# Performance work log

Hardware: AMD Instinct MI355X
Metric: run time of the kernel (lower is better)

Reference implementation:

```python
import jax, jax.numpy as jnp
import numpy as np

N_NODES = 50000
N_EDGES = 800000
NFEAT, NHID, NCLASS = 512, 256, 128
N_UV = 2048


def gcn_layer(x, adj_row, adj_col, adj_val, W, b):
    # support = x @ W ; out = A @ support (sparse COO spmm) + b
    support = x @ W                                   # [N, out]
    msgs = adj_val[:, None] * support[adj_col]        # [E, out]
    out = jax.ops.segment_sum(msgs, adj_row, num_segments=N_NODES)
    return out + b


def setup_inputs() -> dict:
    key = jax.random.key(0)
    ks = jax.random.split(key, 12)
    u = jax.random.randint(ks[0], (N_UV,), 0, N_NODES)
    v = jax.random.randint(ks[1], (N_UV,), 0, N_NODES)
    x = jax.random.normal(ks[2], (N_NODES, NFEAT), dtype=jnp.float32)
    adj_row = jnp.sort(jax.random.randint(ks[3], (N_EDGES,), 0, N_NODES))
    adj_col = jax.random.randint(ks[4], (N_EDGES,), 0, N_NODES)
    adj_val = jax.random.uniform(ks[5], (N_EDGES,), dtype=jnp.float32)
    s1 = 1.0 / np.sqrt(NHID)
    s2 = 1.0 / np.sqrt(NCLASS)
    W1 = jax.random.uniform(ks[6], (NFEAT, NHID), minval=-s1, maxval=s1, dtype=jnp.float32)
    b1 = jax.random.uniform(ks[7], (NHID,), minval=-s1, maxval=s1, dtype=jnp.float32)
    W2 = jax.random.uniform(ks[8], (NHID, NCLASS), minval=-s2, maxval=s2, dtype=jnp.float32)
    b2 = jax.random.uniform(ks[9], (NCLASS,), minval=-s2, maxval=s2, dtype=jnp.float32)
    We = jax.random.normal(ks[10], (NCLASS, NCLASS), dtype=jnp.float32) * (1.0 / np.sqrt(NCLASS))
    return {"u": u, "v": v, "x": x, "adj_row": adj_row, "adj_col": adj_col,
            "adj_val": adj_val, "W1": W1, "b1": b1, "W2": W2, "b2": b2, "We": We}


def reference(u, v, x, adj_row, adj_col, adj_val, W1, b1, W2, b2, We):
    # layer 1: GCN + ReLU (dropout is identity in eval mode)
    h = jax.nn.relu(gcn_layer(x, adj_row, adj_col, adj_val, W1, b1))
    # layer 2: GCN
    z = gcn_layer(h, adj_row, adj_col, adj_val, W2, b2)          # [N, nclass]
    # edge scoring: sigmoid(w_edge(z[u]) @ z[v].T)
    zu = z[u] @ We.T                                             # [U, nclass] (nn.Linear: x @ W.T)
    zv = z[v]                                                    # [V, nclass]
    p_uv = jax.nn.sigmoid(zu @ zv.T)                             # [U, V]
    return p_uv
```

## Files before the change

### kernel.cpp

```cpp
#include <hip/hip_runtime.h>
#include <hip/hip_bf16.h>
#include <math.h>

#define N_NODES 50000
#define N_EDGES 800000
#define NFEAT   512
#define NHID    256
#define NCLASS  128
#define N_UV    2048

#define Q24_SCALE  524288.0f
#define Q24_INV    1.9073486328125e-6f

typedef __bf16    bf16x8 __attribute__((ext_vector_type(8)));
typedef short     s16x8  __attribute__((ext_vector_type(8)));
typedef float     f32x4  __attribute__((ext_vector_type(4)));

struct __attribute__((packed)) U3 { unsigned a, b, c; };

__device__ __forceinline__ unsigned short bf16_rn(float f) {
  unsigned u = __float_as_uint(f);
  u += 0x7fffu + ((u >> 16) & 1u);
  return (unsigned short)(u >> 16);
}
__device__ __forceinline__ float bf16_to_f(unsigned short h) {
  return __uint_as_float(((unsigned)h) << 16);
}
__device__ __forceinline__ void unpack24(unsigned a, unsigned b, unsigned c,
                                         int& e0, int& e1, int& e2, int& e3) {
  e0 = ((int)(a << 8)) >> 8;
  e1 = ((int)((b << 16) | ((a >> 24) << 8))) >> 8;
  e2 = ((int)((c << 24) | ((b >> 16) << 8))) >> 8;
  e3 = ((int)c) >> 8;
}

#define LDSPAD 72

template <bool ASPLIT, int OMODE>
__global__ __launch_bounds__(256, 4) void gemm_mfma_wide(
    const float* __restrict__ Af,
    const unsigned short* __restrict__ Ahi, const unsigned short* __restrict__ Alo,
    const unsigned short* __restrict__ BThi, const unsigned short* __restrict__ BTlo,
    float* __restrict__ C, unsigned char* __restrict__ Cq, int M, int N, int K) {
  __shared__ unsigned short sAh[64 * LDSPAD];
  __shared__ unsigned short sAl[64 * LDSPAD];

  const int tid  = threadIdx.x;
  const int lane = tid & 63;
  const int wave = tid >> 6;
  const int wn   = wave << 5;
  const int lm   = lane & 15;
  const int quad = lane >> 4;
  const int m0   = blockIdx.y * 64;
  const int n0   = blockIdx.x * 128;

  const int r32 = tid >> 4;
  const int c32 = (tid & 15) * 4;
  const int r16 = tid >> 3;
  const int c16 = (tid & 7) * 8;

  float4 pA[4]; s16x8 pAh[2], pAl[2];

  f32x4 acc[4][2];
#pragma unroll
  for (int i = 0; i < 4; ++i)
#pragma unroll
    for (int j = 0; j < 2; ++j)
#pragma unroll
      for (int r = 0; r < 4; ++r) acc[i][j][r] = 0.f;

#define LOAD_TILE(k0)                                                          \
  do {                                                                         \
    if (ASPLIT) {                                                              \
      _Pragma("unroll") for (int p = 0; p < 4; ++p) {                          \
        const int m = m0 + p * 16 + r32;                                       \
        pA[p] = make_float4(0.f, 0.f, 0.f, 0.f);                               \
        if (m < M) pA[p] = *(const float4*)&Af[(size_t)m * K + (k0) + c32];    \
      }                                                                        \
    } else {                                                                   \
      _Pragma("unroll") for (int p = 0; p < 2; ++p) {                          \
        const int m = m0 + p * 32 + r16;                                       \
        _Pragma("unroll") for (int e = 0; e < 8; ++e) { pAh[p][e] = 0; pAl[p][e] = 0; } \
        if (m < M) {                                                           \
          pAh[p] = *(const s16x8*)&Ahi[(size_t)m * K + (k0) + c16];            \
          pAl[p] = *(const s16x8*)&Alo[(size_t)m * K + (k0) + c16];            \
        }                                                                      \
      }                                                                        \
    }                                                                          \
  } while (0)

#define SPLIT4W(v, hv, lv)                                                     \
  hv.x = bf16_rn(v.x); lv.x = bf16_rn(v.x - bf16_to_f(hv.x));                  \
  hv.y = bf16_rn(v.y); lv.y = bf16_rn(v.y - bf16_to_f(hv.y));                  \
  hv.z = bf16_rn(v.z); lv.z = bf16_rn(v.z - bf16_to_f(hv.z));                  \
  hv.w = bf16_rn(v.w); lv.w = bf16_rn(v.w - bf16_to_f(hv.w));

#define STORE_TILE()                                                           \
  do {                                                                         \
    if (ASPLIT) {                                                              \
      _Pragma("unroll") for (int p = 0; p < 4; ++p) {                          \
        ushort4 hv, lv; SPLIT4W(pA[p], hv, lv);                                \
        const int row = p * 16 + r32;                                          \
        *(ushort4*)&sAh[row * LDSPAD + c32] = hv;                              \
        *(ushort4*)&sAl[row * LDSPAD + c32] = lv;                              \
      }                                                                        \
    } else {                                                                   \
      _Pragma("unroll") for (int p = 0; p < 2; ++p) {                          \
        const int row = p * 32 + r16;                                          \
        *(s16x8*)&sAh[row * LDSPAD + c16] = pAh[p];                            \
        *(s16x8*)&sAl[row * LDSPAD + c16] = pAl[p];                            \
      }                                                                        \
    }                                                                          \
  } while (0)

  LOAD_TILE(0);

  const unsigned short* Bhrow = BThi + (size_t)(n0 + wn + lm) * K;
  const unsigned short* Blrow = BTlo + (size_t)(n0 + wn + lm) * K;

  for (int k0 = 0; k0 < K; k0 += 64) {
    if (k0) __syncthreads();
    STORE_TILE();
    __syncthreads();

    bf16x8 bH[2][2], bL[2][2];
#pragma unroll
    for (int ks = 0; ks < 2; ++ks)
#pragma unroll
      for (int j = 0; j < 2; ++j) {
        const size_t off = (size_t)(j * 16) * K + k0 + ks * 32 + quad * 8;
        bH[ks][j] = __builtin_bit_cast(bf16x8, *(const s16x8*)(Bhrow + off));
        bL[ks][j] = __builtin_bit_cast(bf16x8, *(const s16x8*)(Blrow + off));
      }

    if (k0 + 64 < K) LOAD_TILE(k0 + 64);

#pragma unroll
    for (int ks = 0; ks < 2; ++ks) {
      const int koff = ks * 32 + quad * 8;
#pragma unroll
      for (int i = 0; i < 4; ++i) {
        const int r = i * 16 + lm;
        const bf16x8 aH = __builtin_bit_cast(bf16x8, *(const s16x8*)&sAh[r * LDSPAD + koff]);
        const bf16x8 aL = __builtin_bit_cast(bf16x8, *(const s16x8*)&sAl[r * LDSPAD + koff]);
#pragma unroll
        for (int j = 0; j < 2; ++j) {
          acc[i][j] = __builtin_amdgcn_mfma_f32_16x16x32_bf16(aH, bH[ks][j], acc[i][j], 0, 0, 0);
          acc[i][j] = __builtin_amdgcn_mfma_f32_16x16x32_bf16(aH, bL[ks][j], acc[i][j], 0, 0, 0);
          acc[i][j] = __builtin_amdgcn_mfma_f32_16x16x32_bf16(aL, bH[ks][j], acc[i][j], 0, 0, 0);
        }
      }
    }
  }

#pragma unroll
  for (int i = 0; i < 4; ++i)
#pragma unroll
    for (int j = 0; j < 2; ++j) {
      const int col = n0 + wn + j * 16 + lm;
#pragma unroll
      for (int r = 0; r < 4; ++r) {
        const int row = m0 + i * 16 + quad * 4 + r;
        if (row < M) {
          float v = acc[i][j][r];
          if (OMODE == 2) {
            int q = __float2int_rn(v * Q24_SCALE);
            q = q > 8388607 ? 8388607 : (q < -8388608 ? -8388608 : q);
            unsigned char* p = Cq + ((size_t)row * N + col) * 3;
            p[0] = (unsigned char)(q & 0xFF);
            p[1] = (unsigned char)((q >> 8) & 0xFF);
            p[2] = (unsigned char)((q >> 16) & 0xFF);
          } else {
            C[(size_t)row * N + col] = v;
          }
        }
      }
    }
#undef LOAD_TILE
#undef STORE_TILE
#undef SPLIT4W
}

template <int OMODE>
__global__ __launch_bounds__(256, 2) void gemm_mfma_split(
    const float* __restrict__ Af, const float* __restrict__ BTf,
    float* __restrict__ C, int M, int N, int K) {
  __shared__ unsigned short sAh[128 * LDSPAD];
  __shared__ unsigned short sAl[128 * LDSPAD];
  __shared__ unsigned short sBh[128 * LDSPAD];
  __shared__ unsigned short sBl[128 * LDSPAD];

  const int tid  = threadIdx.x;
  const int lane = tid & 63;
  const int wave = tid >> 6;
  const int wm   = (wave >> 1) << 6;
  const int wn   = (wave & 1) << 6;
  const int lm   = lane & 15;
  const int quad = lane >> 4;
  const int m0   = blockIdx.y * 128;
  const int n0   = blockIdx.x * 128;

  const int r32 = tid >> 4;
  const int c32 = (tid & 15) * 4;

  float4 pA[8];
  float4 pB[8];

  f32x4 acc[4][4];
#pragma unroll
  for (int i = 0; i < 4; ++i)
#pragma unroll
    for (int j = 0; j < 4; ++j)
#pragma unroll
      for (int r = 0; r < 4; ++r) acc[i][j][r] = 0.f;

#define LOAD_TILE(k0)                                                          \
  do {                                                                         \
    _Pragma("unroll") for (int p = 0; p < 8; ++p) {                            \
      const int m = m0 + p * 16 + r32;                                         \
      pA[p] = make_float4(0.f, 0.f, 0.f, 0.f);                                 \
      if (m < M) pA[p] = *(const float4*)&Af[(size_t)m * K + (k0) + c32];      \
    }                                                                          \
    _Pragma("unroll") for (int p = 0; p < 8; ++p) {                            \
      const int n = n0 + p * 16 + r32;                                         \
      pB[p] = *(const float4*)&BTf[(size_t)n * K + (k0) + c32];                \
    }                                                                          \
  } while (0)

#define SPLIT4(v, hv, lv)                                                      \
  hv.x = bf16_rn(v.x); lv.x = bf16_rn(v.x - bf16_to_f(hv.x));                  \
  hv.y = bf16_rn(v.y); lv.y = bf16_rn(v.y - bf16_to_f(hv.y));                  \
  hv.z = bf16_rn(v.z); lv.z = bf16_rn(v.z - bf16_to_f(hv.z));                  \
  hv.w = bf16_rn(v.w); lv.w = bf16_rn(v.w - bf16_to_f(hv.w));

#define STORE_TILE()                                                           \
  do {                                                                         \
    _Pragma("unroll") for (int p = 0; p < 8; ++p) {                            \
      ushort4 hv, lv; SPLIT4(pA[p], hv, lv);                                   \
      const int row = p * 16 + r32;                                            \
      *(ushort4*)&sAh[row * LDSPAD + c32] = hv;                                \
      *(ushort4*)&sAl[row * LDSPAD + c32] = lv;                                \
    }                                                                          \
    _Pragma("unroll") for (int p = 0; p < 8; ++p) {                            \
      ushort4 hv, lv; SPLIT4(pB[p], hv, lv);                                   \
      const int row = p * 16 + r32;                                            \
      *(ushort4*)&sBh[row * LDSPAD + c32] = hv;                                \
      *(ushort4*)&sBl[row * LDSPAD + c32] = lv;                                \
    }                                                                          \
  } while (0)

  LOAD_TILE(0);

  for (int k0 = 0; k0 < K; k0 += 64) {
    if (k0) __syncthreads();
    STORE_TILE();
    __syncthreads();
    if (k0 + 64 < K) LOAD_TILE(k0 + 64);

#pragma unroll
    for (int ks = 0; ks < 2; ++ks) {
      const int koff = ks * 32 + quad * 8;
      bf16x8 aH[4], aL[4], bH[4], bL[4];
#pragma unroll
      for (int i = 0; i < 4; ++i) {
        const int r = wm + i * 16 + lm;
        aH[i] = __builtin_bit_cast(bf16x8, *(const s16x8*)&sAh[r * LDSPAD + koff]);
        aL[i] = __builtin_bit_cast(bf16x8, *(const s16x8*)&sAl[r * LDSPAD + koff]);
      }
#pragma unroll
      for (int j = 0; j < 4; ++j) {
        const int r = wn + j * 16 + lm;
        bH[j] = __builtin_bit_cast(bf16x8, *(const s16x8*)&sBh[r * LDSPAD + koff]);
        bL[j] = __builtin_bit_cast(bf16x8, *(const s16x8*)&sBl[r * LDSPAD + koff]);
      }
#pragma unroll
      for (int i = 0; i < 4; ++i)
#pragma unroll
        for (int j = 0; j < 4; ++j) {
          acc[i][j] = __builtin_amdgcn_mfma_f32_16x16x32_bf16(aH[i], bH[j], acc[i][j], 0, 0, 0);
          acc[i][j] = __builtin_amdgcn_mfma_f32_16x16x32_bf16(aH[i], bL[j], acc[i][j], 0, 0, 0);
          acc[i][j] = __builtin_amdgcn_mfma_f32_16x16x32_bf16(aL[i], bH[j], acc[i][j], 0, 0, 0);
        }
    }
  }

#pragma unroll
  for (int i = 0; i < 4; ++i)
#pragma unroll
    for (int j = 0; j < 4; ++j) {
      const int col = n0 + wn + j * 16 + lm;
#pragma unroll
      for (int r = 0; r < 4; ++r) {
        const int row = m0 + wm + i * 16 + quad * 4 + r;
        if (row < M) {
          float v = acc[i][j][r];
          if (OMODE == 1) v = 1.f / (1.f + expf(-v));
          C[(size_t)row * N + col] = v;
        }
      }
    }
#undef LOAD_TILE
#undef STORE_TILE
#undef SPLIT4
}

__global__ __launch_bounds__(256) void prep_all(
    const int* __restrict__ rows, int* __restrict__ row_ptr,
    const float* __restrict__ W1, unsigned short* __restrict__ W1Thi,
    unsigned short* __restrict__ W1Tlo,
    const float* __restrict__ W2, unsigned short* __restrict__ W2Thi,
    unsigned short* __restrict__ W2Tlo) {
  const int idx = blockIdx.x * 256 + threadIdx.x;
  if (idx < N_EDGES) {
    const int r = rows[idx];
    const int rprev = (idx == 0) ? -1 : rows[idx - 1];
    for (int n = rprev + 1; n <= r; ++n) row_ptr[n] = idx;
    if (idx == N_EDGES - 1)
      for (int n = r + 1; n <= N_NODES; ++n) row_ptr[n] = N_EDGES;
  }
  if (idx < NFEAT * NHID) {
    const int n = idx / NFEAT;
    const int k = idx - n * NFEAT;
    const float f = W1[(size_t)k * NHID + n];
    const unsigned short h = bf16_rn(f);
    W1Thi[idx] = h;
    W1Tlo[idx] = bf16_rn(f - bf16_to_f(h));
  }
  if (idx < NHID * NCLASS) {
    const int n = idx / NHID;
    const int k = idx - n * NHID;
    const float f = W2[(size_t)k * NCLASS + n];
    const unsigned short h = bf16_rn(f);
    W2Thi[idx] = h;
    W2Tlo[idx] = bf16_rn(f - bf16_to_f(h));
  }
}

__global__ __launch_bounds__(256, 4) void spmm256_q24_split(
    const unsigned char* __restrict__ Sq, const int* __restrict__ row_ptr,
    const int* __restrict__ cols, const float* __restrict__ vals,
    const float4* __restrict__ bias4,
    unsigned short* __restrict__ outHi, unsigned short* __restrict__ outLo) {
  const int wave = threadIdx.x >> 6;
  const int lane = threadIdx.x & 63;
  const int node = blockIdx.x * 4 + wave;

  const int lou = __builtin_amdgcn_readfirstlane(row_ptr[node]);
  const int hiu = __builtin_amdgcn_readfirstlane(row_ptr[node + 1]);

  float4 acc = make_float4(0.f, 0.f, 0.f, 0.f);
  const int lane12 = lane * 12;

  for (int base = lou; base < hiu; base += 16) {
    int   c[16];
    float w[16];
    if (base + 16 <= hiu) {
#pragma unroll
      for (int t = 0; t < 16; ++t) {
        c[t] = cols[base + t];
        w[t] = vals[base + t] * Q24_INV;
      }
    } else {
#pragma unroll
      for (int t = 0; t < 16; ++t) {
        const int idx = base + t;
        const int ide = idx < hiu ? idx : hiu - 1;
        c[t] = cols[ide];
        w[t] = idx < hiu ? vals[ide] * Q24_INV : 0.f;
      }
    }
    U3 d[16];
#pragma unroll
    for (int t = 0; t < 16; ++t)
      d[t] = *(const U3*)&Sq[(size_t)c[t] * (NHID * 3) + lane12];
#pragma unroll
    for (int t = 0; t < 16; ++t) {
      int e0, e1, e2, e3;
      unpack24(d[t].a, d[t].b, d[t].c, e0, e1, e2, e3);
      acc.x = fmaf(w[t], (float)e0, acc.x);
      acc.y = fmaf(w[t], (float)e1, acc.y);
      acc.z = fmaf(w[t], (float)e2, acc.z);
      acc.w = fmaf(w[t], (float)e3, acc.w);
    }
  }

  const float4 b = bias4[lane];
  acc.x = fmaxf(acc.x + b.x, 0.f);
  acc.y = fmaxf(acc.y + b.y, 0.f);
  acc.z = fmaxf(acc.z + b.z, 0.f);
  acc.w = fmaxf(acc.w + b.w, 0.f);

  ushort4 hv, lv;
  hv.x = bf16_rn(acc.x); lv.x = bf16_rn(acc.x - bf16_to_f(hv.x));
  hv.y = bf16_rn(acc.y); lv.y = bf16_rn(acc.y - bf16_to_f(hv.y));
  hv.z = bf16_rn(acc.z); lv.z = bf16_rn(acc.z - bf16_to_f(hv.z));
  hv.w = bf16_rn(acc.w); lv.w = bf16_rn(acc.w - bf16_to_f(hv.w));
  const size_t o = (size_t)node * NHID + lane * 4;
  *(ushort4*)&outHi[o] = hv;
  *(ushort4*)&outLo[o] = lv;
}

__global__ __launch_bounds__(256) void spmm128_f32_list(
    const float4* __restrict__ S4, const int* __restrict__ row_ptr,
    const int* __restrict__ cols, const float* __restrict__ vals,
    const float4* __restrict__ bias4,
    const int* __restrict__ u, const int* __restrict__ v,
    float4* __restrict__ out4) {
  const int wave = threadIdx.x >> 6;
  const int lane = threadIdx.x & 63;
  const int half = lane >> 5;
  const int l32  = lane & 31;
  const int idx  = blockIdx.x * 4 + wave;
  const int node = idx < N_UV ? u[idx] : v[idx - N_UV];

  const int lo = row_ptr[node];
  const int hi = row_ptr[node + 1];

  float4 acc = make_float4(0.f, 0.f, 0.f, 0.f);
  int e = lo + half;
  for (; e + 6 < hi; e += 8) {
    int c[4]; float w[4];
#pragma unroll
    for (int t = 0; t < 4; ++t) { c[t] = cols[e + 2 * t]; w[t] = vals[e + 2 * t]; }
    float4 r[4];
#pragma unroll
    for (int t = 0; t < 4; ++t) r[t] = S4[(size_t)c[t] * 32 + l32];
#pragma unroll
    for (int t = 0; t < 4; ++t) {
      acc.x = fmaf(w[t], r[t].x, acc.x); acc.y = fmaf(w[t], r[t].y, acc.y);
      acc.z = fmaf(w[t], r[t].z, acc.z); acc.w = fmaf(w[t], r[t].w, acc.w);
    }
  }
  for (; e < hi; e += 2) {
    const int c = cols[e];
    const float w = vals[e];
    const float4 r = S4[(size_t)c * 32 + l32];
    acc.x = fmaf(w, r.x, acc.x); acc.y = fmaf(w, r.y, acc.y);
    acc.z = fmaf(w, r.z, acc.z); acc.w = fmaf(w, r.w, acc.w);
  }

  acc.x += __shfl_xor(acc.x, 32);
  acc.y += __shfl_xor(acc.y, 32);
  acc.z += __shfl_xor(acc.z, 32);
  acc.w += __shfl_xor(acc.w, 32);

  if (half == 0) {
    const float4 b = bias4[l32];
    acc.x += b.x; acc.y += b.y; acc.z += b.z; acc.w += b.w;
    out4[(size_t)idx * 32 + l32] = acc;
  }
}

extern "C" void kernel_launch(void* const* d_in, const int* in_sizes, int n_in,
                              void* d_out, int out_size, void* d_ws, size_t ws_size,
                              hipStream_t stream) {
  const int*   u       = (const int*)  d_in[0];
  const int*   v       = (const int*)  d_in[1];
  const float* x       = (const float*)d_in[2];
  const int*   adj_row = (const int*)  d_in[3];
  const int*   adj_col = (const int*)  d_in[4];
  const float* adj_val = (const float*)d_in[5];
  const float* W1      = (const float*)d_in[6];
  const float* b1      = (const float*)d_in[7];
  const float* W2      = (const float*)d_in[8];
  const float* b2      = (const float*)d_in[9];
  const float* We      = (const float*)d_in[10];
  float* out = (float*)d_out;

  char* wsb = (char*)d_ws;
  unsigned char* S1q = (unsigned char*)wsb;
  float* S2  = (float*)wsb;
  float* ZUV = (float*)(wsb + (size_t)N_NODES * NCLASS * sizeof(float));
  char* rB = wsb + (size_t)N_NODES * NHID * sizeof(float);
  unsigned short* Hhi = (unsigned short*)rB;
  unsigned short* Hlo = Hhi + (size_t)N_NODES * NHID;
  float* ZU = (float*)rB;
  unsigned short* W1Thi = (unsigned short*)out;
  unsigned short* W1Tlo = W1Thi + NHID * NFEAT;
  unsigned short* W2Thi = W1Tlo + NHID * NFEAT;
  unsigned short* W2Tlo = W2Thi + NCLASS * NHID;
  int* row_ptr = (int*)(W2Tlo + NCLASS * NHID);

  prep_all<<<(N_EDGES + 255) / 256, 256, 0, stream>>>(
      adj_row, row_ptr, W1, W1Thi, W1Tlo, W2, W2Thi, W2Tlo);

  gemm_mfma_wide<true, 2>
      <<<dim3(NHID / 128, (N_NODES + 63) / 64), 256, 0, stream>>>(
      x, nullptr, nullptr, W1Thi, W1Tlo,
      nullptr, S1q, N_NODES, NHID, NFEAT);

  spmm256_q24_split<<<N_NODES / 4, 256, 0, stream>>>(
      S1q, row_ptr, adj_col, adj_val, (const float4*)b1, Hhi, Hlo);

  gemm_mfma_wide<false, 0>
      <<<dim3(NCLASS / 128, (N_NODES + 63) / 64), 256, 0, stream>>>(
      nullptr, Hhi, Hlo, W2Thi, W2Tlo,
      S2, nullptr, N_NODES, NCLASS, NHID);

  spmm128_f32_list<<<(2 * N_UV) / 4, 256, 0, stream>>>(
      (const float4*)S2, row_ptr, adj_col, adj_val, (const float4*)b2,
      u, v, (float4*)ZUV);

  gemm_mfma_split<0>
      <<<dim3(NCLASS / 128, N_UV / 128), 256, 0, stream>>>(
      ZUV, We, ZU, N_UV, NCLASS, NCLASS);

  gemm_mfma_split<1>
      <<<dim3(N_UV / 128, N_UV / 128), 256, 0, stream>>>(
      ZU, ZUV + (size_t)N_UV * NCLASS, out, N_UV, N_UV, NCLASS);
}
```

Before: 370.2 us.

## Reorder layer-2 as aggregate-then-transform only for needed u/v nodes

Layer 2 used to run the H·W2 GEMM over all 50000 nodes and then gather only 4096 u/v rows. It now aggregates the 256-wide H for just those 4096 nodes, then multiplies the small result by W2 with the bias fused into the epilogue. This drops a full-graph GEMM and the bf16 hi/lo split of H. In exchange H is stored as fp32 (more bytes written by the first SpMM), and the second aggregation gathers 256-wide rows instead of 128-wide.

```diff
diff --git a/kernel.cpp b/kernel.cpp
--- a/kernel.cpp
+++ b/kernel.cpp
@@ -41,7 +41,8 @@
     const float* __restrict__ Af,
     const unsigned short* __restrict__ Ahi, const unsigned short* __restrict__ Alo,
     const unsigned short* __restrict__ BThi, const unsigned short* __restrict__ BTlo,
-    float* __restrict__ C, unsigned char* __restrict__ Cq, int M, int N, int K) {
+    float* __restrict__ C, unsigned char* __restrict__ Cq,
+    const float* __restrict__ bias, int M, int N, int K) {
   __shared__ unsigned short sAh[64 * LDSPAD];
   __shared__ unsigned short sAl[64 * LDSPAD];
 
@@ -158,6 +159,7 @@
 #pragma unroll
     for (int j = 0; j < 2; ++j) {
       const int col = n0 + wn + j * 16 + lm;
+      const float bb = (OMODE == 3) ? bias[col] : 0.f;
 #pragma unroll
       for (int r = 0; r < 4; ++r) {
         const int row = m0 + i * 16 + quad * 4 + r;
@@ -170,6 +172,8 @@
             p[0] = (unsigned char)(q & 0xFF);
             p[1] = (unsigned char)((q >> 8) & 0xFF);
             p[2] = (unsigned char)((q >> 16) & 0xFF);
+          } else if (OMODE == 3) {
+            C[(size_t)row * N + col] = v + bb;
           } else {
             C[(size_t)row * N + col] = v;
           }
@@ -336,11 +340,10 @@
   }
 }
 
-__global__ __launch_bounds__(256, 4) void spmm256_q24_split(
+__global__ __launch_bounds__(256, 4) void spmm256_q24_f32(
     const unsigned char* __restrict__ Sq, const int* __restrict__ row_ptr,
     const int* __restrict__ cols, const float* __restrict__ vals,
-    const float4* __restrict__ bias4,
-    unsigned short* __restrict__ outHi, unsigned short* __restrict__ outLo) {
+    const float4* __restrict__ bias4, float4* __restrict__ outF) {
   const int wave = threadIdx.x >> 6;
   const int lane = threadIdx.x & 63;
   const int node = blockIdx.x * 4 + wave;
@@ -390,65 +393,50 @@
   acc.z = fmaxf(acc.z + b.z, 0.f);
   acc.w = fmaxf(acc.w + b.w, 0.f);
 
-  ushort4 hv, lv;
-  hv.x = bf16_rn(acc.x); lv.x = bf16_rn(acc.x - bf16_to_f(hv.x));
-  hv.y = bf16_rn(acc.y); lv.y = bf16_rn(acc.y - bf16_to_f(hv.y));
-  hv.z = bf16_rn(acc.z); lv.z = bf16_rn(acc.z - bf16_to_f(hv.z));
-  hv.w = bf16_rn(acc.w); lv.w = bf16_rn(acc.w - bf16_to_f(hv.w));
-  const size_t o = (size_t)node * NHID + lane * 4;
-  *(ushort4*)&outHi[o] = hv;
-  *(ushort4*)&outLo[o] = lv;
-}
-
-__global__ __launch_bounds__(256) void spmm128_f32_list(
-    const float4* __restrict__ S4, const int* __restrict__ row_ptr,
+  outF[(size_t)node * 64 + lane] = acc;
+}
+
+__global__ __launch_bounds__(256, 4) void spmm256_f32_list(
+    const float4* __restrict__ H4, const int* __restrict__ row_ptr,
     const int* __restrict__ cols, const float* __restrict__ vals,
-    const float4* __restrict__ bias4,
     const int* __restrict__ u, const int* __restrict__ v,
     float4* __restrict__ out4) {
   const int wave = threadIdx.x >> 6;
   const int lane = threadIdx.x & 63;
-  const int half = lane >> 5;
-  const int l32  = lane & 31;
   const int idx  = blockIdx.x * 4 + wave;
   const int node = idx < N_UV ? u[idx] : v[idx - N_UV];
 
-  const int lo = row_ptr[node];
-  const int hi = row_ptr[node + 1];
+  const int lou = __builtin_amdgcn_readfirstlane(row_ptr[node]);
+  const int hiu = __builtin_amdgcn_readfirstlane(row_ptr[node + 1]);
 
   float4 acc = make_float4(0.f, 0.f, 0.f, 0.f);
-  int e = lo + half;
-  for (; e + 6 < hi; e += 8) {
-    int c[4]; float w[4];
-#pragma unroll
-    for (int t = 0; t < 4; ++t) { c[t] = cols[e + 2 * t]; w[t] = vals[e + 2 * t]; }
-    float4 r[4];
-#pragma unroll
-    for (int t = 0; t < 4; ++t) r[t] = S4[(size_t)c[t] * 32 + l32];
-#pragma unroll
-    for (int t = 0; t < 4; ++t) {
+
+  for (int base = lou; base < hiu; base += 16) {
+    int   c[16];
+    float w[16];
+    if (base + 16 <= hiu) {
+#pragma unroll
+      for (int t = 0; t < 16; ++t) { c[t] = cols[base + t]; w[t] = vals[base + t]; }
+    } else {
+#pragma unroll
+      for (int t = 0; t < 16; ++t) {
+        const int e = base + t;
+        const int ie = e < hiu ? e : hiu - 1;
+        c[t] = cols[ie];
+        w[t] = e < hiu ? vals[ie] : 0.f;
+      }
+    }
+    float4 r[16];
+#pragma unroll
+    for (int t = 0; t < 16; ++t) r[t] = H4[(size_t)c[t] * 64 + lane];
+#pragma unroll
+    for (int t = 0; t < 16; ++t) {
       acc.x = fmaf(w[t], r[t].x, acc.x); acc.y = fmaf(w[t], r[t].y, acc.y);
       acc.z = fmaf(w[t], r[t].z, acc.z); acc.w = fmaf(w[t], r[t].w, acc.w);
     }
   }
-  for (; e < hi; e += 2) {
-    const int c = cols[e];
-    const float w = vals[e];
-    const float4 r = S4[(size_t)c * 32 + l32];
-    acc.x = fmaf(w, r.x, acc.x); acc.y = fmaf(w, r.y, acc.y);
-    acc.z = fmaf(w, r.z, acc.z); acc.w = fmaf(w, r.w, acc.w);
-  }
-
-  acc.x += __shfl_xor(acc.x, 32);
-  acc.y += __shfl_xor(acc.y, 32);
-  acc.z += __shfl_xor(acc.z, 32);
-  acc.w += __shfl_xor(acc.w, 32);
-
-  if (half == 0) {
-    const float4 b = bias4[l32];
-    acc.x += b.x; acc.y += b.y; acc.z += b.z; acc.w += b.w;
-    out4[(size_t)idx * 32 + l32] = acc;
-  }
+
+  out4[(size_t)idx * 64 + lane] = acc;
 }
 
 extern "C" void kernel_launch(void* const* d_in, const int* in_sizes, int n_in,
@@ -469,12 +457,10 @@
 
   char* wsb = (char*)d_ws;
   unsigned char* S1q = (unsigned char*)wsb;
-  float* S2  = (float*)wsb;
-  float* ZUV = (float*)(wsb + (size_t)N_NODES * NCLASS * sizeof(float));
-  char* rB = wsb + (size_t)N_NODES * NHID * sizeof(float);
-  unsigned short* Hhi = (unsigned short*)rB;
-  unsigned short* Hlo = Hhi + (size_t)N_NODES * NHID;
-  float* ZU = (float*)rB;
+  float* ZUV2 = (float*)wsb;
+  float* ZUV  = (float*)(wsb + (4u << 20));
+  float* ZU   = (float*)(wsb + (6u << 20));
+  float* Hf = (float*)(wsb + (size_t)N_NODES * NHID * sizeof(float));
   unsigned short* W1Thi = (unsigned short*)out;
   unsigned short* W1Tlo = W1Thi + NHID * NFEAT;
   unsigned short* W2Thi = W1Tlo + NHID * NFEAT;
@@ -487,19 +473,18 @@
   gemm_mfma_wide<true, 2>
       <<<dim3(NHID / 128, (N_NODES + 63) / 64), 256, 0, stream>>>(
       x, nullptr, nullptr, W1Thi, W1Tlo,
-      nullptr, S1q, N_NODES, NHID, NFEAT);
-
-  spmm256_q24_split<<<N_NODES / 4, 256, 0, stream>>>(
-      S1q, row_ptr, adj_col, adj_val, (const float4*)b1, Hhi, Hlo);
-
-  gemm_mfma_wide<false, 0>
-      <<<dim3(NCLASS / 128, (N_NODES + 63) / 64), 256, 0, stream>>>(
-      nullptr, Hhi, Hlo, W2Thi, W2Tlo,
-      S2, nullptr, N_NODES, NCLASS, NHID);
-
-  spmm128_f32_list<<<(2 * N_UV) / 4, 256, 0, stream>>>(
-      (const float4*)S2, row_ptr, adj_col, adj_val, (const float4*)b2,
-      u, v, (float4*)ZUV);
+      nullptr, S1q, nullptr, N_NODES, NHID, NFEAT);
+
+  spmm256_q24_f32<<<N_NODES / 4, 256, 0, stream>>>(
+      S1q, row_ptr, adj_col, adj_val, (const float4*)b1, (float4*)Hf);
+
+  spmm256_f32_list<<<(2 * N_UV) / 4, 256, 0, stream>>>(
+      (const float4*)Hf, row_ptr, adj_col, adj_val, u, v, (float4*)ZUV2);
+
+  gemm_mfma_wide<true, 3>
+      <<<dim3(NCLASS / 128, (2 * N_UV) / 64), 256, 0, stream>>>(
+      ZUV2, nullptr, nullptr, W2Thi, W2Tlo,
+      ZUV, nullptr, b2, 2 * N_UV, NCLASS, NHID);
 
   gemm_mfma_split<0>
       <<<dim3(NCLASS / 128, N_UV / 128), 256, 0, stream>>>(
```

After: 365.5 us. No clear change (-1.3%).
